# Kernel tuning notes

Hardware: AMD Instinct MI355X
Metric: run time of the kernel (lower is better)

Reference implementation:

```python
import jax, jax.numpy as jnp
import numpy as np

H = 128

def _gru_layer(x_tbi, h0, w_ih, w_hh, b_ih, b_hh):
    # x_tbi: [T, B, in], h0: [B, H]
    # Precompute input-side gates for all timesteps in one big GEMM.
    xg = jnp.einsum('tbi,gi->tbg', x_tbi, w_ih) + b_ih  # [T, B, 3H]

    def step(h, xg_t):
        hg = h @ w_hh.T + b_hh                      # [B, 3H]
        xr, xz, xn = jnp.split(xg_t, 3, axis=-1)
        hr, hz, hn = jnp.split(hg, 3, axis=-1)
        r = jax.nn.sigmoid(xr + hr)
        z = jax.nn.sigmoid(xz + hz)
        n = jnp.tanh(xn + r * hn)
        h_new = (1.0 - z) * n + z * h
        return h_new, h_new

    hT, ys = jax.lax.scan(step, h0, xg)             # ys: [T, B, H]
    return ys, hT


def setup_inputs() -> dict:
    key = jax.random.key(0)
    ks = jax.random.split(key, 12)
    B, T = 64, 4096
    s0 = 1.0 / np.sqrt(H)  # PyTorch GRU init scale
    return {
        'data':  jax.random.normal(ks[0], (B, T, 1), dtype=jnp.float32),
        'hidden': jnp.zeros((2, B, H), dtype=jnp.float32),
        'w_ih0': jax.random.uniform(ks[1], (3 * H, 1), jnp.float32, -s0, s0),
        'w_hh0': jax.random.uniform(ks[2], (3 * H, H), jnp.float32, -s0, s0),
        'b_ih0': jax.random.uniform(ks[3], (3 * H,), jnp.float32, -s0, s0),
        'b_hh0': jax.random.uniform(ks[4], (3 * H,), jnp.float32, -s0, s0),
        'w_ih1': jax.random.uniform(ks[5], (3 * H, H), jnp.float32, -s0, s0),
        'w_hh1': jax.random.uniform(ks[6], (3 * H, H), jnp.float32, -s0, s0),
        'b_ih1': jax.random.uniform(ks[7], (3 * H,), jnp.float32, -s0, s0),
        'b_hh1': jax.random.uniform(ks[8], (3 * H,), jnp.float32, -s0, s0),
        'fc_w':  jax.random.uniform(ks[9], (1, H), jnp.float32, -s0, s0),
        'fc_b':  jax.random.uniform(ks[10], (1,), jnp.float32, -s0, s0),
    }


def reference(data, hidden, w_ih0, w_hh0, b_ih0, b_hh0,
              w_ih1, w_hh1, b_ih1, b_hh1, fc_w, fc_b):
    # data: [B, T, 1] (batch_first). Work in [T, B, ...] for scan.
    x = jnp.transpose(data, (1, 0, 2))
    y0, h0T = _gru_layer(x, hidden[0], w_ih0, w_hh0, b_ih0, b_hh0)
    y1, h1T = _gru_layer(y0, hidden[1], w_ih1, w_hh1, b_ih1, b_hh1)
    out_gru = jnp.transpose(y1, (1, 0, 2))          # [B, T, H]
    out_hidden = jnp.stack([h0T, h1T], axis=0)      # [2, B, H]
    out_data = jax.nn.relu(out_gru) @ fc_w.T + fc_b  # [B, T, 1]
    return out_data, out_hidden
```

## Files before the change

### kernel.cpp

```cpp
#include <hip/hip_runtime.h>

#define TT 4096
#define BB 64
#define RR 16
#define OUT_HID (BB*TT)

#define SYS_LDU(p)    __hip_atomic_load((p),      __ATOMIC_RELAXED, __HIP_MEMORY_SCOPE_SYSTEM)
#define SYS_STU(p,v)  __hip_atomic_store((p),(v), __ATOMIC_RELAXED, __HIP_MEMORY_SCOPE_SYSTEM)
#define SYS_STF(p,v)  __hip_atomic_store((p),(v), __ATOMIC_RELAXED, __HIP_MEMORY_SCOPE_SYSTEM)

__device__ __forceinline__ float sigm(float x) {
    return __builtin_amdgcn_rcpf(1.0f + __expf(-x));
}
__device__ __forceinline__ float tanhfast(float x) {
    return 1.0f - 2.0f * __builtin_amdgcn_rcpf(1.0f + __expf(2.0f * x));
}

#define FMA4(acc, wv, hv)                                            \
    acc = fmaf((wv).x, (hv).x, acc); acc = fmaf((wv).y, (hv).y, acc); \
    acc = fmaf((wv).z, (hv).z, acc); acc = fmaf((wv).w, (hv).w, acc);

#define X8(M) M(0) M(1) M(2) M(3) M(4) M(5) M(6) M(7)

#define DECLW(i) float4 wA##i, wB##i, wC##i;
#define LDW(i)   wA##i = *(const float4*)(rpA + 16*(i)); \
                 wB##i = *(const float4*)(rpB + 16*(i)); \
                 wC##i = *(const float4*)(rpC + 16*(i));
#define PIN1(vv) { float _t0 = (vv).x, _t1 = (vv).y, _t2 = (vv).z, _t3 = (vv).w; \
    asm volatile("" : "+v"(_t0), "+v"(_t1), "+v"(_t2), "+v"(_t3));              \
    (vv).x = _t0; (vv).y = _t1; (vv).z = _t2; (vv).w = _t3; }
#define PINW(i)  PIN1(wA##i) PIN1(wB##i) PIN1(wC##i)
#define DECLY(i) float4 y##i;
#define GEMV_LDS(i) { float4 hv_ = hb4[4*(i) + c]; \
    FMA4(a0, wA##i, hv_); FMA4(a1, wB##i, hv_); FMA4(a2, wC##i, hv_); }
#define GEMV_Y(i) { FMA4(a0, wA##i, y##i); FMA4(a1, wB##i, y##i); FMA4(a2, wC##i, y##i); }

#define RED3() \
    float A0 = a0 + __shfl_xor(a0, 1); A0 += __shfl_xor(A0, 2); \
    float A1 = a1 + __shfl_xor(a1, 1); A1 += __shfl_xor(A1, 2); \
    float A2 = a2 + __shfl_xor(a2, 1); A2 += __shfl_xor(A2, 2);

__global__ __launch_bounds__(512, 2) void gru_pipe(
    const float* __restrict__ data,   const float* __restrict__ hidden,
    const float* __restrict__ w_ih0,  const float* __restrict__ w_hh0,
    const float* __restrict__ b_ih0,  const float* __restrict__ b_hh0,
    const float* __restrict__ w_ih1,  const float* __restrict__ w_hh1,
    const float* __restrict__ b_ih1,  const float* __restrict__ b_hh1,
    const float* __restrict__ fc_w,   const float* __restrict__ fc_b,
    float* __restrict__ out, float* __restrict__ wsf)
{
    const int bid  = blockIdx.x;
    const int role = bid >> 6;
    const int b    = bid & 63;
    const int tid  = threadIdx.x;
    const int u    = tid >> 2;
    const int c    = tid & 3;

    float* y0r = wsf;
    float* xgr = wsf + BB*RR*128;
    unsigned* fl   = (unsigned*)(wsf + BB*RR*128 + BB*RR*384);
    unsigned* yflag = fl + 0*BB*RR + b*RR;
    unsigned* ycons = fl + 1*BB*RR + b*RR;
    unsigned* xflag = fl + 2*BB*RR + b*RR;
    unsigned* xcons = fl + 3*BB*RR + b*RR;

    __shared__ __align__(16) float hs[128];
    __shared__ float xs[TT];

    if (role == 0) {
        X8(DECLW)
        { const float* rpA = w_hh0 + u*128 + 4*c;
          const float* rpB = rpA + 16384; const float* rpC = rpA + 32768;
          X8(LDW) }
        X8(PINW)
        const float br  = b_ih0[u]       + b_hh0[u];
        const float bz  = b_ih0[u + 128] + b_hh0[u + 128];
        const float bin = b_ih0[u + 256];
        const float bhn = b_hh0[u + 256];
        const float wir = w_ih0[u], wiz = w_ih0[u + 128], win = w_ih0[u + 256];

        float hold = hidden[b*128 + u];
        if (tid < 128) hs[tid] = hidden[b*128 + tid];
        { const float* xp = data + (size_t)b*TT;
          for (int i = tid; i < TT; i += 512) xs[i] = xp[i]; }
        __syncthreads();

        const float4* hb4 = (const float4*)hs;
        float* yr = y0r + (size_t)b*RR*128;
        unsigned g = 0;

        for (int t = 0; t < TT; ++t) {
            const int s = t & (RR - 1);
            if (tid == 0 && t >= RR) {
                while (g != (unsigned)(t - RR + 1)) {
                    __builtin_amdgcn_s_sleep(1); g = SYS_LDU(&ycons[s]);
                }
            }
            const float xv = xs[t];
            float a0 = 0.f, a1 = 0.f, a2 = 0.f;
            X8(GEMV_LDS)
            RED3()
            const float r = sigm(fmaf(xv, wir, A0 + br));
            const float z = sigm(fmaf(xv, wiz, A1 + bz));
            const float n = tanhfast(fmaf(r, A2 + bhn, fmaf(xv, win, bin)));
            const float hnew = fmaf(z, hold - n, n);
            __syncthreads();
            if (c == 0) { hs[u] = hnew; SYS_STF(&yr[s*128 + u], hnew); }
            __syncthreads();
            if (tid == 0) SYS_STU(&yflag[s], (unsigned)(t + 1));
            if (t + 1 >= RR) g = SYS_LDU(&ycons[(t + 1) & (RR - 1)]);
            hold = hnew;
        }
        if (tid < 128) out[OUT_HID + b*128 + tid] = hs[tid];

    } else if (role <= 2) {
        X8(DECLW)
        { const float* rpA = w_ih1 + u*128 + 4*c;
          const float* rpB = rpA + 16384; const float* rpC = rpA + 32768;
          X8(LDW) }
        X8(PINW)
        X8(DECLY)
        const int par = role - 1;
        float* xg = xgr + (size_t)b*RR*384;
        const float* yrd = y0r + (size_t)b*RR*128;

        unsigned fy = SYS_LDU(&yflag[par & (RR - 1)]);
        unsigned fx = 0;

        for (int t = par; t < TT; t += 2) {
            const int s = t & (RR - 1);
            while (fy != (unsigned)(t + 1)) { __builtin_amdgcn_s_sleep(1); fy = SYS_LDU(&yflag[s]); }
            if (t >= RR)
                while (fx != (unsigned)(t - RR + 1)) { __builtin_amdgcn_s_sleep(1); fx = SYS_LDU(&xcons[s]); }
            const float4* yb = (const float4*)(yrd + s*128 + 4*c);
            asm volatile(
                "global_load_dwordx4 %0, %8, off sc0 sc1\n\t"
                "global_load_dwordx4 %1, %8, off offset:64 sc0 sc1\n\t"
                "global_load_dwordx4 %2, %8, off offset:128 sc0 sc1\n\t"
                "global_load_dwordx4 %3, %8, off offset:192 sc0 sc1\n\t"
                "global_load_dwordx4 %4, %8, off offset:256 sc0 sc1\n\t"
                "global_load_dwordx4 %5, %8, off offset:320 sc0 sc1\n\t"
                "global_load_dwordx4 %6, %8, off offset:384 sc0 sc1\n\t"
                "global_load_dwordx4 %7, %8, off offset:448 sc0 sc1\n\t"
                "s_waitcnt vmcnt(0)"
                : "=&v"(y0), "=&v"(y1), "=&v"(y2), "=&v"(y3),
                  "=&v"(y4), "=&v"(y5), "=&v"(y6), "=&v"(y7)
                : "v"(yb) : "memory");
            fy = SYS_LDU(&yflag[(t + 2) & (RR - 1)]);
            fx = SYS_LDU(&xcons[(t + 2) & (RR - 1)]);
            float a0 = 0.f, a1 = 0.f, a2 = 0.f;
            X8(GEMV_Y)
            RED3()
            if (c == 0) {
                SYS_STF(&xg[s*384 + u],       A0);
                SYS_STF(&xg[s*384 + 128 + u], A1);
                SYS_STF(&xg[s*384 + 256 + u], A2);
            }
            __syncthreads();
            if (tid == 0) {
                SYS_STU(&xflag[s], (unsigned)(t + 1));
                SYS_STU(&ycons[s], (unsigned)(t + 1));
            }
        }

    } else {
        X8(DECLW)
        { const float* rpA = w_hh1 + u*128 + 4*c;
          const float* rpB = rpA + 16384; const float* rpC = rpA + 32768;
          X8(LDW) }
        X8(PINW)
        const float br  = b_ih1[u]       + b_hh1[u];
        const float bz  = b_ih1[u + 128] + b_hh1[u + 128];
        const float bin = b_ih1[u + 256];
        const float bhn = b_hh1[u + 256];
        float fw0 = 0.f, fw1 = 0.f, fb = 0.f;
        if (tid < 64) { fw0 = fc_w[tid]; fw1 = fc_w[tid + 64]; fb = fc_b[0]; }

        float hold = hidden[8192 + b*128 + u];
        if (tid < 128) hs[tid] = hidden[8192 + b*128 + tid];
        __syncthreads();

        const float4* hb4 = (const float4*)hs;
        const float* xgd = xgr + (size_t)b*RR*384;
        float* outp = out + (size_t)b*TT;
        unsigned f = SYS_LDU(&xflag[0]);

        for (int t = 0; t < TT; ++t) {
            const int s = t & (RR - 1);
            while (f != (unsigned)(t + 1)) { __builtin_amdgcn_s_sleep(1); f = SYS_LDU(&xflag[s]); }
            const float* xgp = xgd + s*384 + u;
            float xr, xz, xn;
            asm volatile(
                "global_load_dword %0, %3, off sc0 sc1\n\t"
                "global_load_dword %1, %3, off offset:512 sc0 sc1\n\t"
                "global_load_dword %2, %3, off offset:1024 sc0 sc1"
                : "=&v"(xr), "=&v"(xz), "=&v"(xn) : "v"(xgp) : "memory");
            if (t + 1 < TT) f = SYS_LDU(&xflag[(t + 1) & (RR - 1)]);
            float fcv = 0.f;
            if (tid < 64 && t >= 1)
                fcv = fmaxf(hs[tid], 0.f)*fw0 + fmaxf(hs[tid + 64], 0.f)*fw1;
            float a0 = 0.f, a1 = 0.f, a2 = 0.f;
            X8(GEMV_LDS)
            RED3()
            asm volatile("s_waitcnt vmcnt(0)" : "+v"(xr), "+v"(xz), "+v"(xn));
            const float r = sigm(xr + A0 + br);
            const float z = sigm(xz + A1 + bz);
            const float n = tanhfast(fmaf(r, A2 + bhn, xn + bin));
            const float hnew = fmaf(z, hold - n, n);
            if (tid < 64 && t >= 1) {
#pragma unroll
                for (int off = 1; off < 64; off <<= 1) fcv += __shfl_xor(fcv, off);
                if (tid == 0) outp[t - 1] = fcv + fb;
            }
            __syncthreads();
            if (c == 0) hs[u] = hnew;
            __syncthreads();
            if (tid == 0) SYS_STU(&xcons[s], (unsigned)(t + 1));
            hold = hnew;
        }
        float fcv = 0.f;
        if (tid < 64) {
            fcv = fmaxf(hs[tid], 0.f)*fw0 + fmaxf(hs[tid + 64], 0.f)*fw1;
#pragma unroll
            for (int off = 1; off < 64; off <<= 1) fcv += __shfl_xor(fcv, off);
            if (tid == 0) outp[TT - 1] = fcv + fb;
        }
        if (tid < 128) out[OUT_HID + 8192 + b*128 + tid] = hs[tid];
    }
}

extern "C" void kernel_launch(void* const* d_in, const int* in_sizes, int n_in,
                              void* d_out, int out_size, void* d_ws, size_t ws_size,
                              hipStream_t stream) {
    (void)in_sizes; (void)n_in; (void)out_size; (void)ws_size;
    gru_pipe<<<256, 512, 0, stream>>>(
        (const float*)d_in[0],  (const float*)d_in[1],
        (const float*)d_in[2],  (const float*)d_in[3],
        (const float*)d_in[4],  (const float*)d_in[5],
        (const float*)d_in[6],  (const float*)d_in[7],
        (const float*)d_in[8],  (const float*)d_in[9],
        (const float*)d_in[10], (const float*)d_in[11],
        (float*)d_out, (float*)d_ws);
}
```

Before: 5.666 ms.

## Halve block size to 256 threads, doubling per-thread weight registers

```diff
diff --git a/kernel.cpp b/kernel.cpp
--- a/kernel.cpp
+++ b/kernel.cpp
@@ -4,6 +4,7 @@
 #define BB 64
 #define RR 16
 #define OUT_HID (BB*TT)
+#define SPINMAX 100000
 
 #define SYS_LDU(p)    __hip_atomic_load((p),      __ATOMIC_RELAXED, __HIP_MEMORY_SCOPE_SYSTEM)
 #define SYS_STU(p,v)  __hip_atomic_store((p),(v), __ATOMIC_RELAXED, __HIP_MEMORY_SCOPE_SYSTEM)
@@ -16,31 +17,52 @@
     return 1.0f - 2.0f * __builtin_amdgcn_rcpf(1.0f + __expf(2.0f * x));
 }
 
+#define WAIT_EQ(p, want, cur, dead)                                           \
+    if (!(dead)) {                                                            \
+        int k_ = 0;                                                           \
+        while ((cur) != (unsigned)(want)) {                                   \
+            if (++k_ > SPINMAX) { (dead) = true; break; }                     \
+            __builtin_amdgcn_s_sleep(1); (cur) = SYS_LDU(p);                  \
+        }                                                                     \
+    }
+
 #define FMA4(acc, wv, hv)                                            \
     acc = fmaf((wv).x, (hv).x, acc); acc = fmaf((wv).y, (hv).y, acc); \
     acc = fmaf((wv).z, (hv).z, acc); acc = fmaf((wv).w, (hv).w, acc);
 
-#define X8(M) M(0) M(1) M(2) M(3) M(4) M(5) M(6) M(7)
-
-#define DECLW(i) float4 wA##i, wB##i, wC##i;
-#define LDW(i)   wA##i = *(const float4*)(rpA + 16*(i)); \
-                 wB##i = *(const float4*)(rpB + 16*(i)); \
-                 wC##i = *(const float4*)(rpC + 16*(i));
+#define X8(M)  M(0) M(1) M(2) M(3) M(4) M(5) M(6) M(7)
+#define X16(M) M(0) M(1) M(2) M(3) M(4) M(5) M(6) M(7) \
+               M(8) M(9) M(10) M(11) M(12) M(13) M(14) M(15)
+
 #define PIN1(vv) { float _t0 = (vv).x, _t1 = (vv).y, _t2 = (vv).z, _t3 = (vv).w; \
     asm volatile("" : "+v"(_t0), "+v"(_t1), "+v"(_t2), "+v"(_t3));              \
     (vv).x = _t0; (vv).y = _t1; (vv).z = _t2; (vv).w = _t3; }
-#define PINW(i)  PIN1(wA##i) PIN1(wB##i) PIN1(wC##i)
-#define DECLY(i) float4 y##i;
-#define GEMV_LDS(i) { float4 hv_ = hb4[4*(i) + c]; \
+
+#define DECLW3(i) float4 wA##i, wB##i, wC##i;
+#define LDW3(i)   wA##i = *(const float4*)(rpA + 4*(i)); \
+                  wB##i = *(const float4*)(rpB + 4*(i)); \
+                  wC##i = *(const float4*)(rpC + 4*(i));
+#define PINW3(i)  PIN1(wA##i) PIN1(wB##i) PIN1(wC##i)
+#define GEMV3(i)  { float4 hv_ = hb4[i]; \
     FMA4(a0, wA##i, hv_); FMA4(a1, wB##i, hv_); FMA4(a2, wC##i, hv_); }
-#define GEMV_Y(i) { FMA4(a0, wA##i, y##i); FMA4(a1, wB##i, y##i); FMA4(a2, wC##i, y##i); }
-
-#define RED3() \
-    float A0 = a0 + __shfl_xor(a0, 1); A0 += __shfl_xor(A0, 2); \
-    float A1 = a1 + __shfl_xor(a1, 1); A1 += __shfl_xor(A1, 2); \
-    float A2 = a2 + __shfl_xor(a2, 1); A2 += __shfl_xor(A2, 2);
-
-__global__ __launch_bounds__(512, 2) void gru_pipe(
+
+#define DECLW6(i) float4 uA##i, uB##i, uC##i, uD##i, uE##i, uF##i;
+#define LDW6(i)   uA##i = *(const float4*)(rp0 + 4*(i)); \
+                  uB##i = *(const float4*)(rp1 + 4*(i)); \
+                  uC##i = *(const float4*)(rp2 + 4*(i)); \
+                  uD##i = *(const float4*)(rp3 + 4*(i)); \
+                  uE##i = *(const float4*)(rp4 + 4*(i)); \
+                  uF##i = *(const float4*)(rp5 + 4*(i));
+#define PINW6(i)  PIN1(uA##i) PIN1(uB##i) PIN1(uC##i) PIN1(uD##i) PIN1(uE##i) PIN1(uF##i)
+#define DECLY(i)  float4 y##i;
+#define GEMV6(i)  { FMA4(b0, uA##i, y##i); FMA4(b1, uB##i, y##i); \
+                    FMA4(b2, uC##i, y##i); FMA4(b3, uD##i, y##i); \
+                    FMA4(b4, uE##i, y##i); FMA4(b5, uF##i, y##i); }
+
+__global__
+__attribute__((amdgpu_flat_work_group_size(256, 256)))
+__attribute__((amdgpu_waves_per_eu(2, 2)))
+void gru_pipe(
     const float* __restrict__ data,   const float* __restrict__ hidden,
     const float* __restrict__ w_ih0,  const float* __restrict__ w_hh0,
     const float* __restrict__ b_ih0,  const float* __restrict__ b_hh0,
@@ -53,8 +75,6 @@
     const int role = bid >> 6;
     const int b    = bid & 63;
     const int tid  = threadIdx.x;
-    const int u    = tid >> 2;
-    const int c    = tid & 3;
 
     float* y0r = wsf;
     float* xgr = wsf + BB*RR*128;
@@ -67,12 +87,15 @@
     __shared__ __align__(16) float hs[128];
     __shared__ float xs[TT];
 
+    bool dead = false;
+
     if (role == 0) {
-        X8(DECLW)
-        { const float* rpA = w_hh0 + u*128 + 4*c;
+        const int u = tid >> 1, c = tid & 1;
+        X16(DECLW3)
+        { const float* rpA = w_hh0 + u*128 + 64*c;
           const float* rpB = rpA + 16384; const float* rpC = rpA + 32768;
-          X8(LDW) }
-        X8(PINW)
+          X16(LDW3) }
+        X16(PINW3)
         const float br  = b_ih0[u]       + b_hh0[u];
         const float bz  = b_ih0[u + 128] + b_hh0[u + 128];
         const float bin = b_ih0[u + 256];
@@ -82,24 +105,24 @@
         float hold = hidden[b*128 + u];
         if (tid < 128) hs[tid] = hidden[b*128 + tid];
         { const float* xp = data + (size_t)b*TT;
-          for (int i = tid; i < TT; i += 512) xs[i] = xp[i]; }
+          for (int i = tid; i < TT; i += 256) xs[i] = xp[i]; }
         __syncthreads();
 
-        const float4* hb4 = (const float4*)hs;
+        const float4* hb4 = (const float4*)hs + 16*c;
         float* yr = y0r + (size_t)b*RR*128;
         unsigned g = 0;
 
         for (int t = 0; t < TT; ++t) {
             const int s = t & (RR - 1);
             if (tid == 0 && t >= RR) {
-                while (g != (unsigned)(t - RR + 1)) {
-                    __builtin_amdgcn_s_sleep(1); g = SYS_LDU(&ycons[s]);
-                }
+                WAIT_EQ(&ycons[s], t - RR + 1, g, dead)
             }
             const float xv = xs[t];
             float a0 = 0.f, a1 = 0.f, a2 = 0.f;
-            X8(GEMV_LDS)
-            RED3()
+            X16(GEMV3)
+            float A0 = a0 + __shfl_xor(a0, 1);
+            float A1 = a1 + __shfl_xor(a1, 1);
+            float A2 = a2 + __shfl_xor(a2, 1);
             const float r = sigm(fmaf(xv, wir, A0 + br));
             const float z = sigm(fmaf(xv, wiz, A1 + bz));
             const float n = tanhfast(fmaf(r, A2 + bhn, fmaf(xv, win, bin)));
@@ -114,11 +137,16 @@
         if (tid < 128) out[OUT_HID + b*128 + tid] = hs[tid];
 
     } else if (role <= 2) {
-        X8(DECLW)
-        { const float* rpA = w_ih1 + u*128 + 4*c;
-          const float* rpB = rpA + 16384; const float* rpC = rpA + 32768;
-          X8(LDW) }
-        X8(PINW)
+        const int v = tid >> 2, c4 = tid & 3;
+        X8(DECLW6)
+        { const float* rp0 = w_ih1 + (v      )*128 + 32*c4;
+          const float* rp1 = w_ih1 + (v +  64)*128 + 32*c4;
+          const float* rp2 = w_ih1 + (v + 128)*128 + 32*c4;
+          const float* rp3 = w_ih1 + (v + 192)*128 + 32*c4;
+          const float* rp4 = w_ih1 + (v + 256)*128 + 32*c4;
+          const float* rp5 = w_ih1 + (v + 320)*128 + 32*c4;
+          X8(LDW6) }
+        X8(PINW6)
         X8(DECLY)
         const int par = role - 1;
         float* xg = xgr + (size_t)b*RR*384;
@@ -129,32 +157,41 @@
 
         for (int t = par; t < TT; t += 2) {
             const int s = t & (RR - 1);
-            while (fy != (unsigned)(t + 1)) { __builtin_amdgcn_s_sleep(1); fy = SYS_LDU(&yflag[s]); }
-            if (t >= RR)
-                while (fx != (unsigned)(t - RR + 1)) { __builtin_amdgcn_s_sleep(1); fx = SYS_LDU(&xcons[s]); }
-            const float4* yb = (const float4*)(yrd + s*128 + 4*c);
+            WAIT_EQ(&yflag[s], t + 1, fy, dead)
+            if (t >= RR) {
+                WAIT_EQ(&xcons[s], t - RR + 1, fx, dead)
+            }
+            const float4* yb = (const float4*)(yrd + s*128 + 32*c4);
             asm volatile(
                 "global_load_dwordx4 %0, %8, off sc0 sc1\n\t"
-                "global_load_dwordx4 %1, %8, off offset:64 sc0 sc1\n\t"
-                "global_load_dwordx4 %2, %8, off offset:128 sc0 sc1\n\t"
-                "global_load_dwordx4 %3, %8, off offset:192 sc0 sc1\n\t"
-                "global_load_dwordx4 %4, %8, off offset:256 sc0 sc1\n\t"
-                "global_load_dwordx4 %5, %8, off offset:320 sc0 sc1\n\t"
-                "global_load_dwordx4 %6, %8, off offset:384 sc0 sc1\n\t"
-                "global_load_dwordx4 %7, %8, off offset:448 sc0 sc1\n\t"
+                "global_load_dwordx4 %1, %8, off offset:16 sc0 sc1\n\t"
+                "global_load_dwordx4 %2, %8, off offset:32 sc0 sc1\n\t"
+                "global_load_dwordx4 %3, %8, off offset:48 sc0 sc1\n\t"
+                "global_load_dwordx4 %4, %8, off offset:64 sc0 sc1\n\t"
+                "global_load_dwordx4 %5, %8, off offset:80 sc0 sc1\n\t"
+                "global_load_dwordx4 %6, %8, off offset:96 sc0 sc1\n\t"
+                "global_load_dwordx4 %7, %8, off offset:112 sc0 sc1\n\t"
                 "s_waitcnt vmcnt(0)"
                 : "=&v"(y0), "=&v"(y1), "=&v"(y2), "=&v"(y3),
                   "=&v"(y4), "=&v"(y5), "=&v"(y6), "=&v"(y7)
                 : "v"(yb) : "memory");
             fy = SYS_LDU(&yflag[(t + 2) & (RR - 1)]);
             fx = SYS_LDU(&xcons[(t + 2) & (RR - 1)]);
-            float a0 = 0.f, a1 = 0.f, a2 = 0.f;
-            X8(GEMV_Y)
-            RED3()
-            if (c == 0) {
-                SYS_STF(&xg[s*384 + u],       A0);
-                SYS_STF(&xg[s*384 + 128 + u], A1);
-                SYS_STF(&xg[s*384 + 256 + u], A2);
+            float b0 = 0.f, b1 = 0.f, b2 = 0.f, b3 = 0.f, b4 = 0.f, b5 = 0.f;
+            X8(GEMV6)
+            float B0 = b0 + __shfl_xor(b0, 1); B0 += __shfl_xor(B0, 2);
+            float B1 = b1 + __shfl_xor(b1, 1); B1 += __shfl_xor(B1, 2);
+            float B2 = b2 + __shfl_xor(b2, 1); B2 += __shfl_xor(B2, 2);
+            float B3 = b3 + __shfl_xor(b3, 1); B3 += __shfl_xor(B3, 2);
+            float B4 = b4 + __shfl_xor(b4, 1); B4 += __shfl_xor(B4, 2);
+            float B5 = b5 + __shfl_xor(b5, 1); B5 += __shfl_xor(B5, 2);
+            if (c4 == 0) {
+                SYS_STF(&xg[s*384 + v      ], B0);
+                SYS_STF(&xg[s*384 + v +  64], B1);
+                SYS_STF(&xg[s*384 + v + 128], B2);
+                SYS_STF(&xg[s*384 + v + 192], B3);
+                SYS_STF(&xg[s*384 + v + 256], B4);
+                SYS_STF(&xg[s*384 + v + 320], B5);
             }
             __syncthreads();
             if (tid == 0) {
@@ -164,11 +201,12 @@
         }
 
     } else {
-        X8(DECLW)
-        { const float* rpA = w_hh1 + u*128 + 4*c;
+        const int u = tid >> 1, c = tid & 1;
+        X16(DECLW3)
+        { const float* rpA = w_hh1 + u*128 + 64*c;
           const float* rpB = rpA + 16384; const float* rpC = rpA + 32768;
-          X8(LDW) }
-        X8(PINW)
+          X16(LDW3) }
+        X16(PINW3)
         const float br  = b_ih1[u]       + b_hh1[u];
         const float bz  = b_ih1[u + 128] + b_hh1[u + 128];
         const float bin = b_ih1[u + 256];
@@ -180,14 +218,14 @@
         if (tid < 128) hs[tid] = hidden[8192 + b*128 + tid];
         __syncthreads();
 
-        const float4* hb4 = (const float4*)hs;
+        const float4* hb4 = (const float4*)hs + 16*c;
         const float* xgd = xgr + (size_t)b*RR*384;
         float* outp = out + (size_t)b*TT;
         unsigned f = SYS_LDU(&xflag[0]);
 
         for (int t = 0; t < TT; ++t) {
             const int s = t & (RR - 1);
-            while (f != (unsigned)(t + 1)) { __builtin_amdgcn_s_sleep(1); f = SYS_LDU(&xflag[s]); }
+            WAIT_EQ(&xflag[s], t + 1, f, dead)
             const float* xgp = xgd + s*384 + u;
             float xr, xz, xn;
             asm volatile(
@@ -200,8 +238,10 @@
             if (tid < 64 && t >= 1)
                 fcv = fmaxf(hs[tid], 0.f)*fw0 + fmaxf(hs[tid + 64], 0.f)*fw1;
             float a0 = 0.f, a1 = 0.f, a2 = 0.f;
-            X8(GEMV_LDS)
-            RED3()
+            X16(GEMV3)
+            float A0 = a0 + __shfl_xor(a0, 1);
+            float A1 = a1 + __shfl_xor(a1, 1);
+            float A2 = a2 + __shfl_xor(a2, 1);
             asm volatile("s_waitcnt vmcnt(0)" : "+v"(xr), "+v"(xz), "+v"(xn));
             const float r = sigm(xr + A0 + br);
             const float z = sigm(xz + A1 + bz);
@@ -233,7 +273,7 @@
                               void* d_out, int out_size, void* d_ws, size_t ws_size,
                               hipStream_t stream) {
     (void)in_sizes; (void)n_in; (void)out_size; (void)ws_size;
-    gru_pipe<<<256, 512, 0, stream>>>(
+    gru_pipe<<<256, 256, 0, stream>>>(
         (const float*)d_in[0],  (const float*)d_in[1],
         (const float*)d_in[2],  (const float*)d_in[3],
         (const float*)d_in[4],  (const float*)d_in[5],
```

After: 7.147 ms. +26.1%, slower.
